# Performance work log

Hardware: AMD Instinct MI355X
Metric: run time of the kernel (lower is better)

## Reference

```python
import jax, jax.numpy as jnp
import numpy as np

EPS = 1e-5

def _mish(v):
    return v * jnp.tanh(jax.nn.softplus(v))

def _ln(v):
    m = jnp.mean(v, axis=-1, keepdims=True)
    var = jnp.var(v, axis=-1, keepdims=True)
    return (v - m) * jax.lax.rsqrt(var + EPS)

def setup_inputs() -> dict:
    B, S, D, H_HID = 1024, 64, 768, 3072
    key = jax.random.key(0)
    ks = jax.random.split(key, 12)
    s = 0.02  # init scale for weights
    return {
        "x": jax.random.normal(ks[0], (B, S, D), dtype=jnp.float32),
        "c": jax.random.normal(ks[1], (B, D), dtype=jnp.float32),
        "W_mod": jax.random.normal(ks[2], (D, 6 * D), dtype=jnp.float32) * s,
        "b_mod": jax.random.normal(ks[3], (6 * D,), dtype=jnp.float32) * s,
        "W_qkv": jax.random.normal(ks[4], (D, 3 * D), dtype=jnp.float32) * s,
        "b_qkv": jax.random.normal(ks[5], (3 * D,), dtype=jnp.float32) * s,
        "W_out": jax.random.normal(ks[6], (D, D), dtype=jnp.float32) * s,
        "b_out": jax.random.normal(ks[7], (D,), dtype=jnp.float32) * s,
        "W_f1": jax.random.normal(ks[8], (D, H_HID), dtype=jnp.float32) * s,
        "b_f1": jax.random.normal(ks[9], (H_HID,), dtype=jnp.float32) * s,
        "W_f2": jax.random.normal(ks[10], (H_HID, D), dtype=jnp.float32) * s,
        "b_f2": jax.random.normal(ks[11], (D,), dtype=jnp.float32) * s,
    }

def reference(x, c, W_mod, b_mod, W_qkv, b_qkv, W_out, b_out, W_f1, b_f1, W_f2, b_f2):
    B, S, D = x.shape
    num_heads = 12
    head_dim = D // num_heads

    # AdaLN modulation: Mish(c) -> linear -> 6 vectors, broadcast over S
    mod = _mish(c) @ W_mod + b_mod              # [B, 6D]
    mod = mod[:, None, :]                       # [B, 1, 6D]
    shift1, scale1, gate1, shift2, scale2, gate2 = jnp.split(mod, 6, axis=-1)

    # --- attention sub-block ---
    h = _ln(x) * (1.0 + scale1) + shift1        # [B, S, D]
    qkv = (h @ W_qkv + b_qkv).reshape(B, S, 3, num_heads, head_dim)
    q = qkv[:, :, 0].transpose(0, 2, 1, 3)      # [B, H, S, hd]
    k = qkv[:, :, 1].transpose(0, 2, 1, 3)
    v = qkv[:, :, 2].transpose(0, 2, 1, 3)
    attn = jnp.einsum("bhsd,bhtd->bhst", q, k) * (head_dim ** -0.5)
    attn = jax.nn.softmax(attn, axis=-1)
    h = jnp.einsum("bhst,bhtd->bhsd", attn, v)  # [B, H, S, hd]
    h = h.transpose(0, 2, 1, 3).reshape(B, S, D)
    h = h @ W_out + b_out
    x = x + gate1 * h

    # --- FFN sub-block ---
    h = _ln(x) * (1.0 + scale2) + shift2
    h = _mish(h @ W_f1 + b_f1) @ W_f2 + b_f2
    x = x + gate2 * h
    return x
```

## Files before the change

kernel.cpp:

```cpp
#include <hip/hip_runtime.h>

typedef unsigned int uint;
typedef unsigned short ushort;

using bf16x8 = __attribute__((ext_vector_type(8))) short;
using f32x4  = __attribute__((ext_vector_type(4))) float;

#define LOAD16(g, l) __builtin_amdgcn_global_load_lds( \
    (const __attribute__((address_space(1))) void*)(g), \
    (__attribute__((address_space(3))) void*)(l), 16, 0, 0)

__device__ __forceinline__ ushort f2b(float f){
  uint u = __float_as_uint(f);
  u = (u + 0x7FFFu + ((u >> 16) & 1u)) >> 16;
  return (ushort)u;
}
__device__ __forceinline__ float b2f(ushort h){
  return __uint_as_float(((uint)h) << 16);
}
__device__ __forceinline__ float mishf(float v){
  float t = __expf(v);
  float u = t * (t + 2.f);
  float r = u * __builtin_amdgcn_rcpf(u + 2.f);
  return v > 15.f ? v : v * r;
}

__global__ __launch_bounds__(256) void transpose_f32_bf16(
    const float* __restrict__ W, ushort* __restrict__ Wt, int K, int N)
{
  __shared__ float tile[32][33];
  int k0 = blockIdx.x * 32, n0 = blockIdx.y * 32;
  int tx = threadIdx.x & 31, ty = threadIdx.x >> 5;
  #pragma unroll
  for (int r = ty; r < 32; r += 8)
    tile[r][tx] = W[(size_t)(k0 + r) * N + n0 + tx];
  __syncthreads();
  #pragma unroll
  for (int r = ty; r < 32; r += 8)
    Wt[(size_t)(n0 + r) * K + k0 + tx] = f2b(tile[tx][r]);
}

__global__ void mish_to_bf16(const float* __restrict__ in, ushort* __restrict__ out, int n){
  int i = blockIdx.x * blockDim.x + threadIdx.x;
  int stride = gridDim.x * blockDim.x;
  for (; i < n; i += stride) out[i] = f2b(mishf(in[i]));
}

__global__ __launch_bounds__(256) void ln_modulate(
    const float* __restrict__ xin,
    const float* __restrict__ modb,
    ushort* __restrict__ out,
    int shift_off, int scale_off)
{
  int row = blockIdx.x;
  int t = threadIdx.x;
  const float* xr = xin + (size_t)row * 768;
  float v0 = xr[t], v1 = xr[t + 256], v2 = xr[t + 512];
  float s  = v0 + v1 + v2;
  float ss = v0*v0 + v1*v1 + v2*v2;
  #pragma unroll
  for (int off = 32; off > 0; off >>= 1){
    s  += __shfl_down(s, off);
    ss += __shfl_down(ss, off);
  }
  __shared__ float rs[4], rss[4];
  int wave = t >> 6, lane = t & 63;
  if (lane == 0){ rs[wave] = s; rss[wave] = ss; }
  __syncthreads();
  s  = rs[0] + rs[1] + rs[2] + rs[3];
  ss = rss[0] + rss[1] + rss[2] + rss[3];
  float mean = s * (1.f / 768.f);
  float var  = ss * (1.f / 768.f) - mean * mean;
  float rstd = rsqrtf(var + 1e-5f);
  const float* mr = modb + (size_t)(row >> 6) * 4608;
  ushort* orow = out + (size_t)row * 768;
  #pragma unroll
  for (int e = 0; e < 3; e++){
    int n = t + e * 256;
    float xv = (e == 0 ? v0 : (e == 1 ? v1 : v2));
    float sc = 1.f + mr[scale_off + n];
    float sh = mr[shift_off + n];
    orow[n] = f2b((xv - mean) * rstd * sc + sh);
  }
}

template<int MODE>
__global__ __launch_bounds__(256) void gemm_bt(
    const ushort* __restrict__ A,
    const ushort* __restrict__ Bt,
    const float* __restrict__ bias,
    float* __restrict__ out_f,
    ushort* __restrict__ out_h,
    const float* __restrict__ resid,
    const float* __restrict__ gate,
    int M, int N, int K)
{
  __shared__ ushort sA[128 * 32];
  __shared__ ushort sB[128 * 32];
  int tid  = threadIdx.x;
  int lane = tid & 63, wave = tid >> 6;
  int l15  = lane & 15, quad = lane >> 4;
  int m0 = blockIdx.x * 128, n0 = blockIdx.y * 128;
  int wm = (wave & 1) * 64, wn = (wave >> 1) * 64;

  int r0  = wave * 32 + (lane >> 2);
  int r1  = r0 + 16;
  int cs  = lane & 3;
  int kc0 = cs ^ ((r0 >> 1) & 3);
  int kc1 = cs ^ ((r1 >> 1) & 3);
  const ushort* gA0 = A  + (size_t)(m0 + r0) * K + kc0 * 8;
  const ushort* gA1 = A  + (size_t)(m0 + r1) * K + kc1 * 8;
  const ushort* gB0 = Bt + (size_t)(n0 + r0) * K + kc0 * 8;
  const ushort* gB1 = Bt + (size_t)(n0 + r1) * K + kc1 * 8;
  ushort* lA0 = &sA[wave * 1024];
  ushort* lA1 = &sA[wave * 1024 + 512];
  ushort* lB0 = &sB[wave * 1024];
  ushort* lB1 = &sB[wave * 1024 + 512];

  int sw = quad ^ ((l15 >> 1) & 3);
  const ushort* pa = &sA[(wm + l15) * 32 + sw * 8];
  const ushort* pb = &sB[(wn + l15) * 32 + sw * 8];

  f32x4 acc[4][4];
  #pragma unroll
  for (int i = 0; i < 4; i++)
    #pragma unroll
    for (int j = 0; j < 4; j++) acc[i][j] = (f32x4){0.f, 0.f, 0.f, 0.f};

  int nk = K >> 5;
  for (int kt = 0; kt < nk; kt++){
    __syncthreads();
    LOAD16(gA0, lA0); LOAD16(gA1, lA1);
    LOAD16(gB0, lB0); LOAD16(gB1, lB1);
    gA0 += 32; gA1 += 32; gB0 += 32; gB1 += 32;
    __syncthreads();
    bf16x8 af[4], bv[4];
    #pragma unroll
    for (int i = 0; i < 4; i++) af[i] = *(const bf16x8*)(pa + i * 512);
    #pragma unroll
    for (int j = 0; j < 4; j++) bv[j] = *(const bf16x8*)(pb + j * 512);
    #pragma unroll
    for (int i = 0; i < 4; i++)
      #pragma unroll
      for (int j = 0; j < 4; j++)
        acc[i][j] = __builtin_amdgcn_mfma_f32_16x16x32_bf16(af[i], bv[j], acc[i][j], 0, 0, 0);
  }

  float bias_v[4];
  #pragma unroll
  for (int j = 0; j < 4; j++) bias_v[j] = bias[n0 + wn + j * 16 + l15];
  #pragma unroll
  for (int i = 0; i < 4; i++){
    int mb = m0 + wm + i * 16 + quad * 4;
    #pragma unroll
    for (int j = 0; j < 4; j++){
      int n = n0 + wn + j * 16 + l15;
      #pragma unroll
      for (int r = 0; r < 4; r++){
        int m = mb + r;
        float v = acc[i][j][r] + bias_v[j];
        size_t idx = (size_t)m * N + n;
        if (MODE == 0)      out_f[idx] = v;
        else if (MODE == 1) out_h[idx] = f2b(v);
        else if (MODE == 2){
          float g = gate[(size_t)(m >> 6) * 4608 + n];
          out_f[idx] = resid[idx] + g * v;
        } else              out_h[idx] = f2b(mishf(v));
      }
    }
  }
}

__global__ __launch_bounds__(256) void attn64(
    const ushort* __restrict__ qkv,
    ushort* __restrict__ out)
{
  __shared__ float kk[64][68];
  __shared__ float vv[64][68];
  __shared__ float sc[64][65];
  __shared__ float red[2][4][64];
  int bi = blockIdx.x, h = blockIdx.y;
  int t  = threadIdx.x;
  int s4 = t >> 2, p = t & 3;
  size_t rowbase = ((size_t)bi * 64 + s4) * 2304 + h * 64;

  {
    const uint4* kp = (const uint4*)(qkv + rowbase + 768  + p * 16);
    const uint4* vp = (const uint4*)(qkv + rowbase + 1536 + p * 16);
    union { uint4 u; ushort s[8]; } k0, k1, v0, v1;
    k0.u = kp[0]; k1.u = kp[1]; v0.u = vp[0]; v1.u = vp[1];
    #pragma unroll
    for (int e = 0; e < 8; e++){
      kk[s4][p * 16 + e]     = b2f(k0.s[e]);
      kk[s4][p * 16 + 8 + e] = b2f(k1.s[e]);
      vv[s4][p * 16 + e]     = b2f(v0.s[e]);
      vv[s4][p * 16 + 8 + e] = b2f(v1.s[e]);
    }
  }
  float qr[64];
  {
    const uint4* qp = (const uint4*)(qkv + rowbase);
    #pragma unroll
    for (int c = 0; c < 8; c++){
      union { uint4 u; ushort s[8]; } q; q.u = qp[c];
      #pragma unroll
      for (int e = 0; e < 8; e++) qr[c * 8 + e] = b2f(q.s[e]);
    }
  }
  __syncthreads();

  float scr[16]; float mx = -1e30f;
  #pragma unroll
  for (int jj = 0; jj < 16; jj++){
    int j = p * 16 + jj;
    float a = 0.f;
    #pragma unroll
    for (int d = 0; d < 64; d++) a += qr[d] * kk[j][d];
    a *= 0.125f;
    scr[jj] = a; mx = fmaxf(mx, a);
  }
  red[0][p][s4] = mx;
  __syncthreads();
  float rmx = fmaxf(fmaxf(red[0][0][s4], red[0][1][s4]),
                    fmaxf(red[0][2][s4], red[0][3][s4]));
  float sm = 0.f;
  #pragma unroll
  for (int jj = 0; jj < 16; jj++){
    float e = __expf(scr[jj] - rmx);
    sm += e;
    sc[s4][p * 16 + jj] = e;
  }
  red[1][p][s4] = sm;
  __syncthreads();
  float rinv = 1.f / (red[1][0][s4] + red[1][1][s4] + red[1][2][s4] + red[1][3][s4]);

  float o[16];
  #pragma unroll
  for (int e = 0; e < 16; e++) o[e] = 0.f;
  for (int j = 0; j < 64; j++){
    float pj = sc[s4][j];
    #pragma unroll
    for (int e = 0; e < 16; e++) o[e] += pj * vv[j][p * 16 + e];
  }
  ushort* op = out + ((size_t)bi * 64 + s4) * 768 + h * 64 + p * 16;
  #pragma unroll
  for (int e = 0; e < 16; e++) op[e] = f2b(o[e] * rinv);
}

extern "C" void kernel_launch(void* const* d_in, const int* in_sizes, int n_in,
                              void* d_out, int out_size, void* d_ws, size_t ws_size,
                              hipStream_t stream)
{
  (void)in_sizes; (void)n_in; (void)out_size; (void)ws_size;
  const float* x     = (const float*)d_in[0];
  const float* c     = (const float*)d_in[1];
  const float* W_mod = (const float*)d_in[2];
  const float* b_mod = (const float*)d_in[3];
  const float* W_qkv = (const float*)d_in[4];
  const float* b_qkv = (const float*)d_in[5];
  const float* W_out = (const float*)d_in[6];
  const float* b_out = (const float*)d_in[7];
  const float* W_f1  = (const float*)d_in[8];
  const float* b_f1  = (const float*)d_in[9];
  const float* W_f2  = (const float*)d_in[10];
  const float* b_f2  = (const float*)d_in[11];
  float* out = (float*)d_out;

  char* ws = (char*)d_ws;
  size_t off = 0;
  auto alloc = [&](size_t bytes)->char* {
    char* p = ws + off; off += (bytes + 255) & ~(size_t)255; return p;
  };
  ushort* Wb_mod = (ushort*)alloc((size_t)768 * 4608 * 2);
  ushort* Wb_qkv = (ushort*)alloc((size_t)768 * 2304 * 2);
  ushort* Wb_out = (ushort*)alloc((size_t)768 * 768  * 2);
  ushort* Wb_f1  = (ushort*)alloc((size_t)768 * 3072 * 2);
  ushort* Wb_f2  = (ushort*)alloc((size_t)3072 * 768 * 2);
  ushort* c_act  = (ushort*)alloc((size_t)1024 * 768 * 2);
  float*  mod    = (float*) alloc((size_t)1024 * 4608 * 4);
  ushort* bufH   = (ushort*)alloc((size_t)16384 * 768  * 2);
  ushort* bufQKV = (ushort*)alloc((size_t)16384 * 2304 * 2);
  ushort* bufG   = (ushort*)alloc((size_t)16384 * 3072 * 2);

  transpose_f32_bf16<<<dim3(24, 144), 256, 0, stream>>>(W_mod, Wb_mod, 768, 4608);
  transpose_f32_bf16<<<dim3(24, 72),  256, 0, stream>>>(W_qkv, Wb_qkv, 768, 2304);
  transpose_f32_bf16<<<dim3(24, 24),  256, 0, stream>>>(W_out, Wb_out, 768, 768);
  transpose_f32_bf16<<<dim3(24, 96),  256, 0, stream>>>(W_f1,  Wb_f1,  768, 3072);
  transpose_f32_bf16<<<dim3(96, 24),  256, 0, stream>>>(W_f2,  Wb_f2,  3072, 768);
  mish_to_bf16<<<512, 256, 0, stream>>>(c, c_act, 1024 * 768);
  gemm_bt<0><<<dim3(8, 36), 256, 0, stream>>>(c_act, Wb_mod, b_mod, mod, nullptr,
                                              nullptr, nullptr, 1024, 4608, 768);

  for (int ch = 0; ch < 4; ch++){
    int b0 = ch * 256;
    const float* xc   = x   + (size_t)b0 * 64 * 768;
    float*       oc   = out + (size_t)b0 * 64 * 768;
    const float* modc = mod + (size_t)b0 * 4608;

    ln_modulate<<<16384, 256, 0, stream>>>(xc, modc, bufH, 0, 768);
    gemm_bt<1><<<dim3(128, 18), 256, 0, stream>>>(bufH, Wb_qkv, b_qkv, nullptr, bufQKV,
                                                  nullptr, nullptr, 16384, 2304, 768);
    attn64<<<dim3(256, 12), 256, 0, stream>>>(bufQKV, bufH);
    gemm_bt<2><<<dim3(128, 6), 256, 0, stream>>>(bufH, Wb_out, b_out, oc, nullptr,
                                                 xc, modc + 1536, 16384, 768, 768);
    ln_modulate<<<16384, 256, 0, stream>>>(oc, modc, bufH, 2304, 3072);
    gemm_bt<3><<<dim3(128, 24), 256, 0, stream>>>(bufH, Wb_f1, b_f1, nullptr, bufG,
                                                  nullptr, nullptr, 16384, 3072, 768);
    gemm_bt<2><<<dim3(128, 6), 256, 0, stream>>>(bufG, Wb_f2, b_f2, oc, nullptr,
                                                 oc, modc + 3840, 16384, 768, 3072);
  }
}
```

Measured before the change: 2.750 ms.

## Triple-buffer LDS in GEMM mainloop with async global-to-LDS prefetch

```diff
diff --git a/kernel.cpp b/kernel.cpp
--- a/kernel.cpp
+++ b/kernel.cpp
@@ -95,8 +95,8 @@
     const float* __restrict__ gate,
     int M, int N, int K)
 {
-  __shared__ ushort sA[128 * 32];
-  __shared__ ushort sB[128 * 32];
+  __shared__ __align__(16) ushort sA[3 * 4096];
+  __shared__ __align__(16) ushort sB[3 * 4096];
   int tid  = threadIdx.x;
   int lane = tid & 63, wave = tid >> 6;
   int l15  = lane & 15, quad = lane >> 4;
@@ -112,14 +112,11 @@
   const ushort* gA1 = A  + (size_t)(m0 + r1) * K + kc1 * 8;
   const ushort* gB0 = Bt + (size_t)(n0 + r0) * K + kc0 * 8;
   const ushort* gB1 = Bt + (size_t)(n0 + r1) * K + kc1 * 8;
-  ushort* lA0 = &sA[wave * 1024];
-  ushort* lA1 = &sA[wave * 1024 + 512];
-  ushort* lB0 = &sB[wave * 1024];
-  ushort* lB1 = &sB[wave * 1024 + 512];
+  int wofs = wave * 1024;
 
   int sw = quad ^ ((l15 >> 1) & 3);
-  const ushort* pa = &sA[(wm + l15) * 32 + sw * 8];
-  const ushort* pb = &sB[(wn + l15) * 32 + sw * 8];
+  int ra = (wm + l15) * 32 + sw * 8;
+  int rb = (wn + l15) * 32 + sw * 8;
 
   f32x4 acc[4][4];
   #pragma unroll
@@ -128,22 +125,47 @@
     for (int j = 0; j < 4; j++) acc[i][j] = (f32x4){0.f, 0.f, 0.f, 0.f};
 
   int nk = K >> 5;
-  for (int kt = 0; kt < nk; kt++){
-    __syncthreads();
-    LOAD16(gA0, lA0); LOAD16(gA1, lA1);
-    LOAD16(gB0, lB0); LOAD16(gB1, lB1);
-    gA0 += 32; gA1 += 32; gB0 += 32; gB1 += 32;
-    __syncthreads();
+
+  LOAD16(gA0, &sA[wofs]);        LOAD16(gA1, &sA[wofs + 512]);
+  LOAD16(gB0, &sB[wofs]);        LOAD16(gB1, &sB[wofs + 512]);
+  gA0 += 32; gA1 += 32; gB0 += 32; gB1 += 32;
+  LOAD16(gA0, &sA[4096 + wofs]); LOAD16(gA1, &sA[4096 + wofs + 512]);
+  LOAD16(gB0, &sB[4096 + wofs]); LOAD16(gB1, &sB[4096 + wofs + 512]);
+  gA0 += 32; gA1 += 32; gB0 += 32; gB1 += 32;
+  asm volatile("s_waitcnt vmcnt(4)" ::: "memory");
+  __builtin_amdgcn_s_barrier();
+
+  int rd = 0;
+  int wr = 2;
+  for (int s = 0; s < nk; s++){
+    if (s + 2 < nk){
+      LOAD16(gA0, &sA[wr * 4096 + wofs]);
+      LOAD16(gA1, &sA[wr * 4096 + wofs + 512]);
+      LOAD16(gB0, &sB[wr * 4096 + wofs]);
+      LOAD16(gB1, &sB[wr * 4096 + wofs + 512]);
+      gA0 += 32; gA1 += 32; gB0 += 32; gB1 += 32;
+    }
+
     bf16x8 af[4], bv[4];
+    const ushort* pa = &sA[rd * 4096 + ra];
+    const ushort* pb = &sB[rd * 4096 + rb];
     #pragma unroll
     for (int i = 0; i < 4; i++) af[i] = *(const bf16x8*)(pa + i * 512);
     #pragma unroll
     for (int j = 0; j < 4; j++) bv[j] = *(const bf16x8*)(pb + j * 512);
+    __builtin_amdgcn_s_setprio(1);
     #pragma unroll
     for (int i = 0; i < 4; i++)
       #pragma unroll
       for (int j = 0; j < 4; j++)
         acc[i][j] = __builtin_amdgcn_mfma_f32_16x16x32_bf16(af[i], bv[j], acc[i][j], 0, 0, 0);
+    __builtin_amdgcn_s_setprio(0);
+
+    if (s + 2 < nk)      asm volatile("s_waitcnt vmcnt(4)" ::: "memory");
+    else if (s + 1 < nk) asm volatile("s_waitcnt vmcnt(0)" ::: "memory");
+    __builtin_amdgcn_s_barrier();
+    rd = (rd == 2) ? 0 : rd + 1;
+    wr = (wr == 2) ? 0 : wr + 1;
   }
 
   float bias_v[4];
```

Measured after the change: 2.661 ms. 3.3% less time.
